# Performance work log

Measured on AMD Instinct MI355X. Metric: run time of the kernel, lower is better.

The kernel has to match this reference:

```python
import jax, jax.numpy as jnp
import numpy as np
import math

B, S, DIM, H = 4, 1024, 4096, 32
HD = DIM // H  # head_dim = 128
MAX_B, MAX_S = 4, 1024
START_POS = 0
ROPE_THETA = 10000.0


def setup_inputs() -> dict:
    key = jax.random.key(0)
    ks = jax.random.split(key, 6)
    x = jax.random.normal(ks[0], (B, S, DIM), dtype=jnp.float32)
    # real RoPE frequencies: freqs_cis[t, j] = exp(i * t * theta^{-2j/hd})
    inv_freq = 1.0 / (ROPE_THETA ** (jnp.arange(0, HD, 2, dtype=jnp.float32) / HD))  # [HD/2]
    t = jnp.arange(START_POS, START_POS + S, dtype=jnp.float32)
    ang = jnp.outer(t, inv_freq)  # [S, HD/2]
    freqs_cos = jnp.cos(ang)
    freqs_sin = jnp.sin(ang)
    # additive causal mask as in llama: -inf above diagonal offset start_pos+1
    mask = jnp.triu(jnp.full((1, 1, S, S), float('-inf'), dtype=jnp.float32), k=START_POS + 1)
    scale = 0.02
    wq = jax.random.normal(ks[1], (DIM, DIM), dtype=jnp.float32) * scale
    wk = jax.random.normal(ks[2], (DIM, DIM), dtype=jnp.float32) * scale
    wv = jax.random.normal(ks[3], (DIM, DIM), dtype=jnp.float32) * scale
    wo = jax.random.normal(ks[4], (DIM, DIM), dtype=jnp.float32) * scale
    cache_k = jnp.zeros((MAX_B, MAX_S, H, HD), dtype=jnp.float32)
    cache_v = jnp.zeros((MAX_B, MAX_S, H, HD), dtype=jnp.float32)
    return {"x": x, "start_pos": START_POS, "freqs_cos": freqs_cos, "freqs_sin": freqs_sin,
            "mask": mask, "wq": wq, "wk": wk, "wv": wv, "wo": wo,
            "cache_k": cache_k, "cache_v": cache_v}


def _apply_rotary(t, cos, sin):
    # t: [B, S, H, HD]; interpret last dim as HD/2 complex pairs (real, imag)
    b, s, h, d = t.shape
    tr = t.reshape(b, s, h, d // 2, 2)
    a, bb = tr[..., 0], tr[..., 1]
    c = cos[None, :, None, :]  # [1, S, 1, HD/2]
    si = sin[None, :, None, :]
    out_r = a * c - bb * si
    out_i = a * si + bb * c
    return jnp.stack([out_r, out_i], axis=-1).reshape(b, s, h, d)


def reference(x, start_pos, freqs_cos, freqs_sin, mask, wq, wk, wv, wo, cache_k, cache_v):
    bsz, seqlen, dim = x.shape
    hd = HD
    # torch Linear: y = x @ W.T, W is [out, in]
    xq = (x @ wq.T).reshape(bsz, seqlen, H, hd)
    xk = (x @ wk.T).reshape(bsz, seqlen, H, hd)
    xv = (x @ wv.T).reshape(bsz, seqlen, H, hd)
    xq = _apply_rotary(xq, freqs_cos, freqs_sin)
    xk = _apply_rotary(xk, freqs_cos, freqs_sin)
    # KV-cache write
    cache_k = jax.lax.dynamic_update_slice(cache_k, xk, (0, start_pos, 0, 0))
    cache_v = jax.lax.dynamic_update_slice(cache_v, xv, (0, start_pos, 0, 0))
    keys = cache_k[:bsz, :start_pos + seqlen]    # [B, K, H, HD]
    values = cache_v[:bsz, :start_pos + seqlen]  # [B, K, H, HD]
    # naive attention: full score matrix
    scores = jnp.einsum('bqhd,bkhd->bhqk', xq, keys) / math.sqrt(hd)
    scores = scores + mask
    probs = jax.nn.softmax(scores.astype(jnp.float32), axis=-1).astype(xq.dtype)
    out = jnp.einsum('bhqk,bkhd->bqhd', probs, values)
    out = out.reshape(bsz, seqlen, -1)
    return out @ wo.T
```

## Files before the change

### kernel.cpp

```cpp
#include <hip/hip_runtime.h>
#include <hip/hip_bf16.h>
#include <cstdint>

typedef __hip_bfloat16 bf16;
typedef __attribute__((ext_vector_type(8))) short frag8;
typedef __attribute__((ext_vector_type(4))) float f32x4;

#define DEV __device__ __forceinline__

DEV void gl_lds16(const void* g, void* l) {
  __builtin_amdgcn_global_load_lds(
      (const __attribute__((address_space(1))) void*)g,
      (__attribute__((address_space(3))) void*)l, 16, 0, 0);
}

DEV void storeC(float* C, size_t idx, float v) { C[idx] = v; }
DEV void storeC(bf16* C, size_t idx, float v) { C[idx] = __float2bfloat16(v); }

__global__ __launch_bounds__(256) void conv_kernel(const float* __restrict__ in,
                                                   bf16* __restrict__ out, int n8) {
  int i = blockIdx.x * 256 + threadIdx.x;
  if (i >= n8) return;
  const float4* in4 = reinterpret_cast<const float4*>(in);
  float4 a = in4[2 * i], b = in4[2 * i + 1];
  union { frag8 v; bf16 h[8]; } u;
  u.h[0] = __float2bfloat16(a.x); u.h[1] = __float2bfloat16(a.y);
  u.h[2] = __float2bfloat16(a.z); u.h[3] = __float2bfloat16(a.w);
  u.h[4] = __float2bfloat16(b.x); u.h[5] = __float2bfloat16(b.y);
  u.h[6] = __float2bfloat16(b.z); u.h[7] = __float2bfloat16(b.w);
  *reinterpret_cast<frag8*>(out + (size_t)i * 8) = u.v;
}

#define MF(a, b, c) __builtin_amdgcn_mfma_f32_16x16x32_bf16(a, b, c, 0, 0, 0)

#define STAGE(isB, h, tt, bp) do {                                             \
    char* _d = lds + ((isB) * 65536) + ((((bp) * 2) + (h)) << 14);             \
    gl_lds16(((isB) ? gB : gA)[h][0] + (size_t)(tt) * 64, _d + ldsOff0);       \
    gl_lds16(((isB) ? gB : gA)[h][1] + (size_t)(tt) * 64, _d + ldsOff1);       \
  } while (0)

#define RDA(mi, ckk) (*(const frag8*)(ab + aRowB + (mi) * 2048 + (ckk)))
#define RDB(ni, ckk) (*(const frag8*)(bb + bRowB + (ni) * 2048 + (ckk)))

#define PHASE(p, SSTAGE, SWAIT) do {                                           \
    if ((p) == 0) {                                                            \
      b00 = RDB(0, ck0); b01 = RDB(0, ck1); b10 = RDB(1, ck0); b11 = RDB(1, ck1); \
      b20 = RDB(2, ck0); b21 = RDB(2, ck1); b30 = RDB(3, ck0); b31 = RDB(3, ck1); \
    }                                                                          \
    frag8 a00 = RDA(2 * (p), ck0), a01 = RDA(2 * (p), ck1);                    \
    frag8 a10 = RDA(2 * (p) + 1, ck0), a11 = RDA(2 * (p) + 1, ck1);            \
    SSTAGE;                                                                    \
    SWAIT;                                                                     \
    __builtin_amdgcn_s_barrier();                                              \
    __builtin_amdgcn_s_setprio(1);                                             \
    acc[2*(p)][0]   = MF(a00, b00, acc[2*(p)][0]);                             \
    acc[2*(p)][1]   = MF(a00, b10, acc[2*(p)][1]);                             \
    acc[2*(p)][2]   = MF(a00, b20, acc[2*(p)][2]);                             \
    acc[2*(p)][3]   = MF(a00, b30, acc[2*(p)][3]);                             \
    acc[2*(p)+1][0] = MF(a10, b00, acc[2*(p)+1][0]);                           \
    acc[2*(p)+1][1] = MF(a10, b10, acc[2*(p)+1][1]);                           \
    acc[2*(p)+1][2] = MF(a10, b20, acc[2*(p)+1][2]);                           \
    acc[2*(p)+1][3] = MF(a10, b30, acc[2*(p)+1][3]);                           \
    acc[2*(p)][0]   = MF(a01, b01, acc[2*(p)][0]);                             \
    acc[2*(p)][1]   = MF(a01, b11, acc[2*(p)][1]);                             \
    acc[2*(p)][2]   = MF(a01, b21, acc[2*(p)][2]);                             \
    acc[2*(p)][3]   = MF(a01, b31, acc[2*(p)][3]);                             \
    acc[2*(p)+1][0] = MF(a11, b01, acc[2*(p)+1][0]);                           \
    acc[2*(p)+1][1] = MF(a11, b11, acc[2*(p)+1][1]);                           \
    acc[2*(p)+1][2] = MF(a11, b21, acc[2*(p)+1][2]);                           \
    acc[2*(p)+1][3] = MF(a11, b31, acc[2*(p)+1][3]);                           \
    __builtin_amdgcn_s_setprio(0);                                             \
    __builtin_amdgcn_s_barrier();                                              \
  } while (0)

#define VM4 asm volatile("s_waitcnt vmcnt(4)" ::: "memory")
#define VM0 asm volatile("s_waitcnt vmcnt(0)" ::: "memory")
#define NOW ((void)0)

#define TILE(t, SA, SB, SWAIT) do {                                            \
    const int _bp2 = ((t) & 1) * 2;                                            \
    char* ab = lds + ((_bp2 + wm) << 14);                                      \
    char* bb = lds + 65536 + ((_bp2 + bhalf) << 14);                           \
    PHASE(0, { if (SA) STAGE(0, 0, (t) + 1, ((t) + 1) & 1); }, NOW);           \
    PHASE(1, { if (SA) STAGE(0, 1, (t) + 1, ((t) + 1) & 1); }, NOW);           \
    PHASE(2, { if (SB) STAGE(1, 0, (t) + 2, (t) & 1); }, NOW);                 \
    PHASE(3, { if (SB) STAGE(1, 1, (t) + 2, (t) & 1); }, SWAIT);               \
  } while (0)

template <typename OutT, int EPI>
__global__ __launch_bounds__(512, 2) void gemm8(const bf16* __restrict__ A,
                                                const bf16* __restrict__ Bt,
                                                OutT* __restrict__ C,
                                                const float* __restrict__ fc,
                                                const float* __restrict__ fs) {
  __shared__ __align__(16) char lds[131072];
  const int K = 4096, N = 4096;
  const int t = threadIdx.x;
  const int lane = t & 63, w = t >> 6;
  const int wm = w >> 2, wn = w & 3;
  const int lr = lane & 15, lg = lane >> 4;
  const int bhalf = wn >> 1;

  const int bid = blockIdx.x;
  const int wg = (bid & 7) * 32 + (bid >> 3);
  const int m0 = (wg >> 4) * 256, n0 = (wg & 15) * 256;

  const bf16* gA[2][2];
  const bf16* gB[2][2];
  int ldsOff0, ldsOff1;
  {
    int c0 = (w * 2 + 0) * 64 + lane;
    int c1 = (w * 2 + 1) * 64 + lane;
    int r0 = c0 >> 3, r1 = c1 >> 3;
    int e0 = ((c0 & 7) ^ (r0 & 7)) * 8;
    int e1 = ((c1 & 7) ^ (r1 & 7)) * 8;
    ldsOff0 = c0 * 16; ldsOff1 = c1 * 16;
    gA[0][0] = A + (size_t)(m0 + r0) * K + e0;
    gA[0][1] = A + (size_t)(m0 + r1) * K + e1;
    gA[1][0] = A + (size_t)(m0 + 128 + r0) * K + e0;
    gA[1][1] = A + (size_t)(m0 + 128 + r1) * K + e1;
    gB[0][0] = Bt + (size_t)(n0 + r0) * K + e0;
    gB[0][1] = Bt + (size_t)(n0 + r1) * K + e1;
    gB[1][0] = Bt + (size_t)(n0 + 128 + r0) * K + e0;
    gB[1][1] = Bt + (size_t)(n0 + 128 + r1) * K + e1;
  }

  const int swz = (lr & 7) << 4;
  const int ck0 = (lg * 16) ^ swz;
  const int ck1 = (64 + lg * 16) ^ swz;
  const int aRowB = lr * 128;
  const int bRowB = ((wn & 1) * 64 + lr) * 128;

  f32x4 acc[8][4];
#pragma unroll
  for (int mi = 0; mi < 8; ++mi)
#pragma unroll
    for (int ni = 0; ni < 4; ++ni) acc[mi][ni] = (f32x4){0.f, 0.f, 0.f, 0.f};

  frag8 b00, b01, b10, b11, b20, b21, b30, b31;

  STAGE(1, 0, 0, 0); STAGE(1, 1, 0, 0);
  STAGE(0, 0, 0, 0); STAGE(0, 1, 0, 0);
  STAGE(1, 0, 1, 1); STAGE(1, 1, 1, 1);
  VM4;
  __builtin_amdgcn_s_barrier();

  for (int tt = 0; tt < 62; tt += 2) {
    TILE(tt, 1, 1, VM4);
    TILE(tt + 1, 1, 1, VM4);
  }
  TILE(62, 1, 0, VM0);
  TILE(63, 0, 0, NOW);

#pragma unroll
  for (int mi = 0; mi < 8; ++mi)
#pragma unroll
    for (int ni = 0; ni < 4; ++ni) {
      f32x4 v = acc[mi][ni];
      int col = n0 + wn * 64 + ni * 16 + lr;
      if (EPI == 1) {
        int i = (col & 127) >> 1;
        const bool odd = (col & 1);
#pragma unroll
        for (int ii = 0; ii < 4; ++ii) {
          int row = m0 + wm * 128 + mi * 16 + lg * 4 + ii;
          int s = row & 1023;
          float c = fc[s * 64 + i], si = fs[s * 64 + i];
          float val = v[ii];
          float par = __shfl_xor(val, 1);
          float o = val * c + (odd ? par * si : -par * si);
          storeC(C, (size_t)row * N + col, o);
        }
      } else if (EPI == 2) {
        int row0 = m0 + wm * 128 + mi * 16 + lg * 4;
        size_t base = ((size_t)(row0 >> 10) * 4096 + col) * 1024 + (row0 & 1023);
        union { ushort4 s4; unsigned short us[4]; } pk;
#pragma unroll
        for (int ii = 0; ii < 4; ++ii) {
          union { bf16 b; unsigned short u; } cv;
          cv.b = __float2bfloat16(v[ii]);
          pk.us[ii] = cv.u;
        }
        *reinterpret_cast<ushort4*>(reinterpret_cast<bf16*>(C) + base) = pk.s4;
      } else {
#pragma unroll
        for (int ii = 0; ii < 4; ++ii) {
          int row = m0 + wm * 128 + mi * 16 + lg * 4 + ii;
          storeC(C, (size_t)row * N + col, v[ii]);
        }
      }
    }
}

__global__ __launch_bounds__(512, 4) void attn_kernel(const bf16* __restrict__ q,
                                                      const bf16* __restrict__ k,
                                                      const bf16* __restrict__ vt,
                                                      bf16* __restrict__ out) {
  __shared__ __align__(16) char als[98304];
  const int qt = blockIdx.x, h = blockIdx.y, b = blockIdx.z;
  const int t = threadIdx.x;
  const int lane = t & 63, w = t >> 6;
  const int lr = lane & 15, lg = lane >> 4;
  const int NT = 2 * qt + 2;

  frag8 aq[4];
  {
    const bf16* qp = q + ((size_t)(b * 1024 + qt * 128 + w * 16 + lr)) * 4096 + h * 128 + lg * 8;
#pragma unroll
    for (int ks = 0; ks < 4; ++ks) aq[ks] = *reinterpret_cast<const frag8*>(qp + ks * 32);
  }

  const bf16* kbase = k + (size_t)b * 1024 * 4096 + h * 128;
  const bf16* vbase = vt + ((size_t)(b * 32 + h)) * 128 * 1024;

  const int L0 = t * 16, L1 = (t + 512) * 16;
  const int kr0 = L0 >> 8, kr1 = L1 >> 8;
  const size_t kOff0 = (size_t)kr0 * 4096 + (((L0 & 255) ^ ((kr0 & 7) << 4)) >> 1);
  const size_t kOff1 = (size_t)kr1 * 4096 + (((L1 & 255) ^ ((kr1 & 7) << 4)) >> 1);
  const int vr0 = L0 >> 7, vr1 = L1 >> 7;
  const size_t vOff0 = (size_t)vr0 * 1024 + (((L0 & 127) ^ ((vr0 & 7) << 4)) >> 1);
  const size_t vOff1 = (size_t)vr1 * 1024 + (((L1 & 127) ^ ((vr1 & 7) << 4)) >> 1);

#define STAGE_K(tt) do { char* _d = als + ((tt) & 1) * 16384;                  \
    gl_lds16(kbase + (size_t)(tt) * 262144 + kOff0, _d + L0);                  \
    gl_lds16(kbase + (size_t)(tt) * 262144 + kOff1, _d + L1); } while (0)
#define STAGE_V(tt) do { char* _d = als + 32768 + ((tt) % 3) * 16384;          \
    gl_lds16(vbase + (size_t)(tt) * 64 + vOff0, _d + L0);                      \
    gl_lds16(vbase + (size_t)(tt) * 64 + vOff1, _d + L1); } while (0)

  f32x4 oacc[8] = {};
  float mrow = -1e30f, lrow = 0.f;
  char* Pw = als + 81920 + w * 2048;
  const float scale = 0.08838834764831845f;
  const int qmaxw = qt * 128 + w * 16 + 15;
  const int qr_g = qt * 128 + w * 16 + lr;

  STAGE_K(0); STAGE_V(0);
  STAGE_K(1); STAGE_V(1);

  for (int kt = 0; kt < NT; ++kt) {
    const bool act = (kt * 64 <= qmaxw);
    const bool domask = (kt >= 2 * qt);
    char* Kc = als + (kt & 1) * 16384;
    char* Vc = als + 32768 + (kt % 3) * 16384;

    if (kt + 1 < NT) { VM4; } else { VM0; }
    __builtin_amdgcn_s_barrier();

    f32x4 sacc[4] = {};
    if (act) {
      __builtin_amdgcn_s_setprio(1);
#pragma unroll
      for (int ks = 0; ks < 4; ++ks) {
#pragma unroll
        for (int ni = 0; ni < 4; ++ni) {
          int n = ni * 16 + lr;
          frag8 bk = *reinterpret_cast<const frag8*>(
              Kc + n * 256 + ((ks * 64 + lg * 16) ^ ((n & 7) << 4)));
          sacc[ni] = MF(bk, aq[ks], sacc[ni]);
        }
      }
      __builtin_amdgcn_s_setprio(0);
    }
    __builtin_amdgcn_s_barrier();
    if (kt + 2 < NT) { STAGE_K(kt + 2); STAGE_V(kt + 2); }

    if (act) {
#pragma unroll
      for (int ni = 0; ni < 4; ++ni)
#pragma unroll
        for (int i = 0; i < 4; ++i) {
          float x = sacc[ni][i] * scale;
          if (domask) {
            int kc = kt * 64 + ni * 16 + lg * 4 + i;
            if (kc > qr_g) x = -1e30f;
          }
          sacc[ni][i] = x;
        }

      float pm = sacc[0][0];
#pragma unroll
      for (int ni = 0; ni < 4; ++ni)
#pragma unroll
        for (int i = 0; i < 4; ++i) pm = fmaxf(pm, sacc[ni][i]);
      pm = fmaxf(pm, __shfl_xor(pm, 16));
      pm = fmaxf(pm, __shfl_xor(pm, 32));
      float mn = fmaxf(mrow, pm);
      float f = __expf(mrow - mn);
      float rs = 0.f;
#pragma unroll
      for (int ni = 0; ni < 4; ++ni)
#pragma unroll
        for (int i = 0; i < 4; ++i) {
          float p = __expf(sacc[ni][i] - mn);
          sacc[ni][i] = p;
          rs += p;
        }
      rs += __shfl_xor(rs, 16);
      rs += __shfl_xor(rs, 32);
      lrow = lrow * f + rs;
      mrow = mn;

#pragma unroll
      for (int ni = 0; ni < 4; ++ni)
#pragma unroll
        for (int jj = 0; jj < 2; ++jj) {
          union { uint32_t u; bf16 hh[2]; } pk;
          pk.hh[0] = __float2bfloat16(sacc[ni][2 * jj]);
          pk.hh[1] = __float2bfloat16(sacc[ni][2 * jj + 1]);
          int kc2 = (ni * 16 + lg * 4 + 2 * jj) * 2;
          *reinterpret_cast<uint32_t*>(Pw + lr * 128 + (kc2 ^ ((lr & 7) << 4))) = pk.u;
        }

      float fi0 = __shfl(f, lg * 4 + 0);
      float fi1 = __shfl(f, lg * 4 + 1);
      float fi2 = __shfl(f, lg * 4 + 2);
      float fi3 = __shfl(f, lg * 4 + 3);
#pragma unroll
      for (int nj = 0; nj < 8; ++nj) {
        oacc[nj][0] *= fi0; oacc[nj][1] *= fi1;
        oacc[nj][2] *= fi2; oacc[nj][3] *= fi3;
      }

      __builtin_amdgcn_s_setprio(1);
#pragma unroll
      for (int ks2 = 0; ks2 < 2; ++ks2) {
        frag8 ap = *reinterpret_cast<const frag8*>(
            Pw + lr * 128 + ((ks2 * 64 + lg * 16) ^ ((lr & 7) << 4)));
#pragma unroll
        for (int nj = 0; nj < 8; ++nj) {
          int d = nj * 16 + lr;
          frag8 bv = *reinterpret_cast<const frag8*>(
              Vc + d * 128 + ((ks2 * 64 + lg * 16) ^ ((d & 7) << 4)));
          oacc[nj] = MF(ap, bv, oacc[nj]);
        }
      }
      __builtin_amdgcn_s_setprio(0);
    }
  }

  float lv0 = __shfl(lrow, lg * 4 + 0);
  float lv1 = __shfl(lrow, lg * 4 + 1);
  float lv2 = __shfl(lrow, lg * 4 + 2);
  float lv3 = __shfl(lrow, lg * 4 + 3);
#pragma unroll
  for (int nj = 0; nj < 8; ++nj) {
    int srow0 = qt * 128 + w * 16 + lg * 4;
    size_t base = ((size_t)(b * 1024 + srow0)) * 4096 + h * 128 + nj * 16 + lr;
    out[base]          = __float2bfloat16(oacc[nj][0] / lv0);
    out[base + 4096]   = __float2bfloat16(oacc[nj][1] / lv1);
    out[base + 8192]   = __float2bfloat16(oacc[nj][2] / lv2);
    out[base + 12288]  = __float2bfloat16(oacc[nj][3] / lv3);
  }
#undef STAGE_K
#undef STAGE_V
}

extern "C" void kernel_launch(void* const* d_in, const int* in_sizes, int n_in,
                              void* d_out, int out_size, void* d_ws, size_t ws_size,
                              hipStream_t stream) {
  const float* x  = (const float*)d_in[0];
  const float* fc = (const float*)d_in[2];
  const float* fs = (const float*)d_in[3];
  const float* wq = (const float*)d_in[5];
  const float* wk = (const float*)d_in[6];
  const float* wv = (const float*)d_in[7];
  const float* wo = (const float*)d_in[8];
  float* out = (float*)d_out;

  const size_t SZ = (size_t)4096 * 4096 * 2;
  char* w = (char*)d_ws;
  bf16* xb  = (bf16*)(w);
  bf16* wb  = (bf16*)(w + SZ);
  bf16* qb  = (bf16*)(w + 2 * SZ);
  bf16* kb  = (bf16*)(w + 3 * SZ);
  bf16* vtb = (bf16*)(w + 4 * SZ);
  bf16* ao  = xb;

  const int n8 = 4096 * 4096 / 8;
  dim3 cgrd(n8 / 256), blk(256);
  dim3 ggrd(256);
  dim3 gblk(512);

  conv_kernel<<<cgrd, blk, 0, stream>>>(x, xb, n8);
  conv_kernel<<<cgrd, blk, 0, stream>>>(wq, wb, n8);
  gemm8<bf16, 1><<<ggrd, gblk, 0, stream>>>(xb, wb, qb, fc, fs);
  conv_kernel<<<cgrd, blk, 0, stream>>>(wk, wb, n8);
  gemm8<bf16, 1><<<ggrd, gblk, 0, stream>>>(xb, wb, kb, fc, fs);
  conv_kernel<<<cgrd, blk, 0, stream>>>(wv, wb, n8);
  gemm8<bf16, 2><<<ggrd, gblk, 0, stream>>>(xb, wb, vtb, fc, fs);
  attn_kernel<<<dim3(8, 32, 4), gblk, 0, stream>>>(qb, kb, vtb, ao);
  conv_kernel<<<cgrd, blk, 0, stream>>>(wo, wb, n8);
  gemm8<float, 0><<<ggrd, gblk, 0, stream>>>(ao, wb, out, fc, fs);
}
```

Measured before the change: 694.6 us.

## Shrink attention query tile to 64 rows and read V directly from global

The attention kernel now uses 256-thread blocks that each handle 64 query rows instead of 128. The grid doubles and LDS per block drops from 96KB to 40KB, which allows higher occupancy and removes the inactive-warp branches on diagonal tiles. V fragments are now loaded straight from global memory inside the PV MFMA loop rather than staged through a triple-buffered LDS tile. This cuts LDS use and staging traffic, at the cost of exposed global-load latency and duplicated V reads across warps and blocks.

Measured after the change: 794.3 us. +14.3%, slower.

```diff
diff --git a/kernel.cpp b/kernel.cpp
--- a/kernel.cpp
+++ b/kernel.cpp
@@ -192,20 +192,20 @@
     }
 }
 
-__global__ __launch_bounds__(512, 4) void attn_kernel(const bf16* __restrict__ q,
+__global__ __launch_bounds__(256, 4) void attn_kernel(const bf16* __restrict__ q,
                                                       const bf16* __restrict__ k,
                                                       const bf16* __restrict__ vt,
                                                       bf16* __restrict__ out) {
-  __shared__ __align__(16) char als[98304];
+  __shared__ __align__(16) char als[40960];
   const int qt = blockIdx.x, h = blockIdx.y, b = blockIdx.z;
   const int t = threadIdx.x;
   const int lane = t & 63, w = t >> 6;
   const int lr = lane & 15, lg = lane >> 4;
-  const int NT = 2 * qt + 2;
+  const int NT = qt + 1;
 
   frag8 aq[4];
   {
-    const bf16* qp = q + ((size_t)(b * 1024 + qt * 128 + w * 16 + lr)) * 4096 + h * 128 + lg * 8;
+    const bf16* qp = q + ((size_t)(b * 1024 + qt * 64 + w * 16 + lr)) * 4096 + h * 128 + lg * 8;
 #pragma unroll
     for (int ks = 0; ks < 4; ++ks) aq[ks] = *reinterpret_cast<const frag8*>(qp + ks * 32);
   }
@@ -213,130 +213,123 @@
   const bf16* kbase = k + (size_t)b * 1024 * 4096 + h * 128;
   const bf16* vbase = vt + ((size_t)(b * 32 + h)) * 128 * 1024;
 
-  const int L0 = t * 16, L1 = (t + 512) * 16;
-  const int kr0 = L0 >> 8, kr1 = L1 >> 8;
-  const size_t kOff0 = (size_t)kr0 * 4096 + (((L0 & 255) ^ ((kr0 & 7) << 4)) >> 1);
-  const size_t kOff1 = (size_t)kr1 * 4096 + (((L1 & 255) ^ ((kr1 & 7) << 4)) >> 1);
-  const int vr0 = L0 >> 7, vr1 = L1 >> 7;
-  const size_t vOff0 = (size_t)vr0 * 1024 + (((L0 & 127) ^ ((vr0 & 7) << 4)) >> 1);
-  const size_t vOff1 = (size_t)vr1 * 1024 + (((L1 & 127) ^ ((vr1 & 7) << 4)) >> 1);
+  size_t kOff[4];
+  int Lc[4];
+#pragma unroll
+  for (int c = 0; c < 4; ++c) {
+    int L = (t + c * 256) * 16;
+    int kr = L >> 8;
+    kOff[c] = (size_t)kr * 4096 + (((L & 255) ^ ((kr & 7) << 4)) >> 1);
+    Lc[c] = L;
+  }
 
 #define STAGE_K(tt) do { char* _d = als + ((tt) & 1) * 16384;                  \
-    gl_lds16(kbase + (size_t)(tt) * 262144 + kOff0, _d + L0);                  \
-    gl_lds16(kbase + (size_t)(tt) * 262144 + kOff1, _d + L1); } while (0)
-#define STAGE_V(tt) do { char* _d = als + 32768 + ((tt) % 3) * 16384;          \
-    gl_lds16(vbase + (size_t)(tt) * 64 + vOff0, _d + L0);                      \
-    gl_lds16(vbase + (size_t)(tt) * 64 + vOff1, _d + L1); } while (0)
+    gl_lds16(kbase + (size_t)(tt) * 262144 + kOff[0], _d + Lc[0]);             \
+    gl_lds16(kbase + (size_t)(tt) * 262144 + kOff[1], _d + Lc[1]);             \
+    gl_lds16(kbase + (size_t)(tt) * 262144 + kOff[2], _d + Lc[2]);             \
+    gl_lds16(kbase + (size_t)(tt) * 262144 + kOff[3], _d + Lc[3]); } while (0)
 
   f32x4 oacc[8] = {};
   float mrow = -1e30f, lrow = 0.f;
-  char* Pw = als + 81920 + w * 2048;
+  char* Pw = als + 32768 + w * 2048;
   const float scale = 0.08838834764831845f;
-  const int qmaxw = qt * 128 + w * 16 + 15;
-  const int qr_g = qt * 128 + w * 16 + lr;
-
-  STAGE_K(0); STAGE_V(0);
-  STAGE_K(1); STAGE_V(1);
+  const int qr_g = qt * 64 + w * 16 + lr;
+
+  STAGE_K(0);
+  STAGE_K(1);
 
   for (int kt = 0; kt < NT; ++kt) {
-    const bool act = (kt * 64 <= qmaxw);
-    const bool domask = (kt >= 2 * qt);
+    const bool domask = (kt == qt);
     char* Kc = als + (kt & 1) * 16384;
-    char* Vc = als + 32768 + (kt % 3) * 16384;
 
     if (kt + 1 < NT) { VM4; } else { VM0; }
     __builtin_amdgcn_s_barrier();
 
     f32x4 sacc[4] = {};
-    if (act) {
-      __builtin_amdgcn_s_setprio(1);
-#pragma unroll
-      for (int ks = 0; ks < 4; ++ks) {
-#pragma unroll
-        for (int ni = 0; ni < 4; ++ni) {
-          int n = ni * 16 + lr;
-          frag8 bk = *reinterpret_cast<const frag8*>(
-              Kc + n * 256 + ((ks * 64 + lg * 16) ^ ((n & 7) << 4)));
-          sacc[ni] = MF(bk, aq[ks], sacc[ni]);
+    __builtin_amdgcn_s_setprio(1);
+#pragma unroll
+    for (int ks = 0; ks < 4; ++ks) {
+#pragma unroll
+      for (int ni = 0; ni < 4; ++ni) {
+        int n = ni * 16 + lr;
+        frag8 bk = *reinterpret_cast<const frag8*>(
+            Kc + n * 256 + ((ks * 64 + lg * 16) ^ ((n & 7) << 4)));
+        sacc[ni] = MF(bk, aq[ks], sacc[ni]);
+      }
+    }
+    __builtin_amdgcn_s_setprio(0);
+    __builtin_amdgcn_s_barrier();
+    if (kt + 2 < NT) STAGE_K(kt + 2);
+
+#pragma unroll
+    for (int ni = 0; ni < 4; ++ni)
+#pragma unroll
+      for (int i = 0; i < 4; ++i) {
+        float x = sacc[ni][i] * scale;
+        if (domask) {
+          int kc = kt * 64 + ni * 16 + lg * 4 + i;
+          if (kc > qr_g) x = -1e30f;
         }
-      }
-      __builtin_amdgcn_s_setprio(0);
+        sacc[ni][i] = x;
+      }
+
+    float pm = sacc[0][0];
+#pragma unroll
+    for (int ni = 0; ni < 4; ++ni)
+#pragma unroll
+      for (int i = 0; i < 4; ++i) pm = fmaxf(pm, sacc[ni][i]);
+    pm = fmaxf(pm, __shfl_xor(pm, 16));
+    pm = fmaxf(pm, __shfl_xor(pm, 32));
+    float mn = fmaxf(mrow, pm);
+    float f = __expf(mrow - mn);
+    float rs = 0.f;
+#pragma unroll
+    for (int ni = 0; ni < 4; ++ni)
+#pragma unroll
+      for (int i = 0; i < 4; ++i) {
+        float p = __expf(sacc[ni][i] - mn);
+        sacc[ni][i] = p;
+        rs += p;
+      }
+    rs += __shfl_xor(rs, 16);
+    rs += __shfl_xor(rs, 32);
+    lrow = lrow * f + rs;
+    mrow = mn;
+
+#pragma unroll
+    for (int ni = 0; ni < 4; ++ni)
+#pragma unroll
+      for (int jj = 0; jj < 2; ++jj) {
+        union { uint32_t u; bf16 hh[2]; } pk;
+        pk.hh[0] = __float2bfloat16(sacc[ni][2 * jj]);
+        pk.hh[1] = __float2bfloat16(sacc[ni][2 * jj + 1]);
+        int kc2 = (ni * 16 + lg * 4 + 2 * jj) * 2;
+        *reinterpret_cast<uint32_t*>(Pw + lr * 128 + (kc2 ^ ((lr & 7) << 4))) = pk.u;
+      }
+
+    float fi0 = __shfl(f, lg * 4 + 0);
+    float fi1 = __shfl(f, lg * 4 + 1);
+    float fi2 = __shfl(f, lg * 4 + 2);
+    float fi3 = __shfl(f, lg * 4 + 3);
+#pragma unroll
+    for (int nj = 0; nj < 8; ++nj) {
+      oacc[nj][0] *= fi0; oacc[nj][1] *= fi1;
+      oacc[nj][2] *= fi2; oacc[nj][3] *= fi3;
     }
-    __builtin_amdgcn_s_barrier();
-    if (kt + 2 < NT) { STAGE_K(kt + 2); STAGE_V(kt + 2); }
-
-    if (act) {
-#pragma unroll
-      for (int ni = 0; ni < 4; ++ni)
-#pragma unroll
-        for (int i = 0; i < 4; ++i) {
-          float x = sacc[ni][i] * scale;
-          if (domask) {
-            int kc = kt * 64 + ni * 16 + lg * 4 + i;
-            if (kc > qr_g) x = -1e30f;
-          }
-          sacc[ni][i] = x;
-        }
-
-      float pm = sacc[0][0];
-#pragma unroll
-      for (int ni = 0; ni < 4; ++ni)
-#pragma unroll
-        for (int i = 0; i < 4; ++i) pm = fmaxf(pm, sacc[ni][i]);
-      pm = fmaxf(pm, __shfl_xor(pm, 16));
-      pm = fmaxf(pm, __shfl_xor(pm, 32));
-      float mn = fmaxf(mrow, pm);
-      float f = __expf(mrow - mn);
-      float rs = 0.f;
-#pragma unroll
-      for (int ni = 0; ni < 4; ++ni)
-#pragma unroll
-        for (int i = 0; i < 4; ++i) {
-          float p = __expf(sacc[ni][i] - mn);
-          sacc[ni][i] = p;
-          rs += p;
-        }
-      rs += __shfl_xor(rs, 16);
-      rs += __shfl_xor(rs, 32);
-      lrow = lrow * f + rs;
-      mrow = mn;
-
-#pragma unroll
-      for (int ni = 0; ni < 4; ++ni)
-#pragma unroll
-        for (int jj = 0; jj < 2; ++jj) {
-          union { uint32_t u; bf16 hh[2]; } pk;
-          pk.hh[0] = __float2bfloat16(sacc[ni][2 * jj]);
-          pk.hh[1] = __float2bfloat16(sacc[ni][2 * jj + 1]);
-          int kc2 = (ni * 16 + lg * 4 + 2 * jj) * 2;
-          *reinterpret_cast<uint32_t*>(Pw + lr * 128 + (kc2 ^ ((lr & 7) << 4))) = pk.u;
-        }
-
-      float fi0 = __shfl(f, lg * 4 + 0);
-      float fi1 = __shfl(f, lg * 4 + 1);
-      float fi2 = __shfl(f, lg * 4 + 2);
-      float fi3 = __shfl(f, lg * 4 + 3);
+
+    __builtin_amdgcn_s_setprio(1);
+#pragma unroll
+    for (int ks2 = 0; ks2 < 2; ++ks2) {
+      frag8 ap = *reinterpret_cast<const frag8*>(
+          Pw + lr * 128 + ((ks2 * 64 + lg * 16) ^ ((lr & 7) << 4)));
 #pragma unroll
       for (int nj = 0; nj < 8; ++nj) {
-        oacc[nj][0] *= fi0; oacc[nj][1] *= fi1;
-        oacc[nj][2] *= fi2; oacc[nj][3] *= fi3;
-      }
-
-      __builtin_amdgcn_s_setprio(1);
-#pragma unroll
-      for (int ks2 = 0; ks2 < 2; ++ks2) {
-        frag8 ap = *reinterpret_cast<const frag8*>(
-            Pw + lr * 128 + ((ks2 * 64 + lg * 16) ^ ((lr & 7) << 4)));
-#pragma unroll
-        for (int nj = 0; nj < 8; ++nj) {
-          int d = nj * 16 + lr;
-          frag8 bv = *reinterpret_cast<const frag8*>(
-              Vc + d * 128 + ((ks2 * 64 + lg * 16) ^ ((d & 7) << 4)));
-          oacc[nj] = MF(ap, bv, oacc[nj]);
-        }
-      }
-      __builtin_amdgcn_s_setprio(0);
+        const bf16* vp = vbase + (size_t)(nj * 16 + lr) * 1024 + kt * 64 + ks2 * 32 + lg * 8;
+        frag8 bv = *reinterpret_cast<const frag8*>(vp);
+        oacc[nj] = MF(ap, bv, oacc[nj]);
+      }
     }
+    __builtin_amdgcn_s_setprio(0);
   }
 
   float lv0 = __shfl(lrow, lg * 4 + 0);
@@ -345,7 +338,7 @@
   float lv3 = __shfl(lrow, lg * 4 + 3);
 #pragma unroll
   for (int nj = 0; nj < 8; ++nj) {
-    int srow0 = qt * 128 + w * 16 + lg * 4;
+    int srow0 = qt * 64 + w * 16 + lg * 4;
     size_t base = ((size_t)(b * 1024 + srow0)) * 4096 + h * 128 + nj * 16 + lr;
     out[base]          = __float2bfloat16(oacc[nj][0] / lv0);
     out[base + 4096]   = __float2bfloat16(oacc[nj][1] / lv1);
@@ -353,7 +346,6 @@
     out[base + 12288]  = __float2bfloat16(oacc[nj][3] / lv3);
   }
 #undef STAGE_K
-#undef STAGE_V
 }
 
 extern "C" void kernel_launch(void* const* d_in, const int* in_sizes, int n_in,
@@ -389,7 +381,7 @@
   gemm8<bf16, 1><<<ggrd, gblk, 0, stream>>>(xb, wb, kb, fc, fs);
   conv_kernel<<<cgrd, blk, 0, stream>>>(wv, wb, n8);
   gemm8<bf16, 2><<<ggrd, gblk, 0, stream>>>(xb, wb, vtb, fc, fs);
-  attn_kernel<<<dim3(8, 32, 4), gblk, 0, stream>>>(qb, kb, vtb, ao);
+  attn_kernel<<<dim3(16, 32, 4), blk, 0, stream>>>(qb, kb, vtb, ao);
   conv_kernel<<<cgrd, blk, 0, stream>>>(wo, wb, n8);
   gemm8<float, 0><<<ggrd, gblk, 0, stream>>>(ao, wb, out, fc, fs);
 }
```

## Fold softmax scale into Q epilogue, lazy rescale, reverse tile order in attention

Applied to the files above, without the earlier changes.

The 1/sqrt(hd) score scale moves into the Q projection's RoPE epilogue, so the attention inner loop no longer multiplies every score. The online softmax skips updating the running max and rescaling the accumulator when no lane's new max exceeds the old one by more than a threshold. This is the lazy-rescale trick and is exact because the final normalisation uses the same stale max. Query tiles launch in reverse order so the longest causal blocks start first. V staging moves from triple to double buffering behind an extra barrier, which frees LDS but adds a synchronisation per iteration.

After: 641.8 us. 1.08x faster.

```diff
diff --git a/kernel.cpp b/kernel.cpp
--- a/kernel.cpp
+++ b/kernel.cpp
@@ -92,7 +92,8 @@
                                                 const bf16* __restrict__ Bt,
                                                 OutT* __restrict__ C,
                                                 const float* __restrict__ fc,
-                                                const float* __restrict__ fs) {
+                                                const float* __restrict__ fs,
+                                                float oscale) {
   __shared__ __align__(16) char lds[131072];
   const int K = 4096, N = 4096;
   const int t = threadIdx.x;
@@ -168,7 +169,7 @@
           float c = fc[s * 64 + i], si = fs[s * 64 + i];
           float val = v[ii];
           float par = __shfl_xor(val, 1);
-          float o = val * c + (odd ? par * si : -par * si);
+          float o = (val * c + (odd ? par * si : -par * si)) * oscale;
           storeC(C, (size_t)row * N + col, o);
         }
       } else if (EPI == 2) {
@@ -196,8 +197,8 @@
                                                       const bf16* __restrict__ k,
                                                       const bf16* __restrict__ vt,
                                                       bf16* __restrict__ out) {
-  __shared__ __align__(16) char als[98304];
-  const int qt = blockIdx.x, h = blockIdx.y, b = blockIdx.z;
+  __shared__ __align__(16) char als[81920];
+  const int qt = 7 - blockIdx.x, h = blockIdx.y, b = blockIdx.z;
   const int t = threadIdx.x;
   const int lane = t & 63, w = t >> 6;
   const int lr = lane & 15, lg = lane >> 4;
@@ -221,28 +222,28 @@
   const size_t vOff0 = (size_t)vr0 * 1024 + (((L0 & 127) ^ ((vr0 & 7) << 4)) >> 1);
   const size_t vOff1 = (size_t)vr1 * 1024 + (((L1 & 127) ^ ((vr1 & 7) << 4)) >> 1);
 
-#define STAGE_K(tt) do { char* _d = als + ((tt) & 1) * 16384;                  \
+#define STAGE_K(tt, bp) do { char* _d = als + (bp) * 16384;                    \
     gl_lds16(kbase + (size_t)(tt) * 262144 + kOff0, _d + L0);                  \
     gl_lds16(kbase + (size_t)(tt) * 262144 + kOff1, _d + L1); } while (0)
-#define STAGE_V(tt) do { char* _d = als + 32768 + ((tt) % 3) * 16384;          \
+#define STAGE_V(tt, bp) do { char* _d = als + 32768 + (bp) * 16384;            \
     gl_lds16(vbase + (size_t)(tt) * 64 + vOff0, _d + L0);                      \
     gl_lds16(vbase + (size_t)(tt) * 64 + vOff1, _d + L1); } while (0)
 
   f32x4 oacc[8] = {};
   float mrow = -1e30f, lrow = 0.f;
-  char* Pw = als + 81920 + w * 2048;
-  const float scale = 0.08838834764831845f;
+  char* Pw = als + 65536 + w * 2048;
   const int qmaxw = qt * 128 + w * 16 + 15;
   const int qr_g = qt * 128 + w * 16 + lr;
 
-  STAGE_K(0); STAGE_V(0);
-  STAGE_K(1); STAGE_V(1);
+  STAGE_K(0, 0); STAGE_V(0, 0);
+  STAGE_K(1, 1); STAGE_V(1, 1);
 
   for (int kt = 0; kt < NT; ++kt) {
+    const int cur = kt & 1;
     const bool act = (kt * 64 <= qmaxw);
     const bool domask = (kt >= 2 * qt);
-    char* Kc = als + (kt & 1) * 16384;
-    char* Vc = als + 32768 + (kt % 3) * 16384;
+    char* Kc = als + cur * 16384;
+    char* Vc = als + 32768 + cur * 16384;
 
     if (kt + 1 < NT) { VM4; } else { VM0; }
     __builtin_amdgcn_s_barrier();
@@ -263,20 +264,18 @@
       __builtin_amdgcn_s_setprio(0);
     }
     __builtin_amdgcn_s_barrier();
-    if (kt + 2 < NT) { STAGE_K(kt + 2); STAGE_V(kt + 2); }
+    if (kt + 2 < NT) STAGE_K(kt + 2, cur);
 
     if (act) {
-#pragma unroll
-      for (int ni = 0; ni < 4; ++ni)
-#pragma unroll
-        for (int i = 0; i < 4; ++i) {
-          float x = sacc[ni][i] * scale;
-          if (domask) {
+      if (domask) {
+#pragma unroll
+        for (int ni = 0; ni < 4; ++ni)
+#pragma unroll
+          for (int i = 0; i < 4; ++i) {
             int kc = kt * 64 + ni * 16 + lg * 4 + i;
-            if (kc > qr_g) x = -1e30f;
+            if (kc > qr_g) sacc[ni][i] = -1e30f;
           }
-          sacc[ni][i] = x;
-        }
+      }
 
       float pm = sacc[0][0];
 #pragma unroll
@@ -285,8 +284,10 @@
         for (int i = 0; i < 4; ++i) pm = fmaxf(pm, sacc[ni][i]);
       pm = fmaxf(pm, __shfl_xor(pm, 16));
       pm = fmaxf(pm, __shfl_xor(pm, 32));
-      float mn = fmaxf(mrow, pm);
-      float f = __expf(mrow - mn);
+      const bool skip = __all(pm <= mrow + 8.f);
+      float mn, f;
+      if (skip) { mn = mrow; f = 1.f; }
+      else      { mn = fmaxf(mrow, pm); f = __expf(mrow - mn); mrow = mn; }
       float rs = 0.f;
 #pragma unroll
       for (int ni = 0; ni < 4; ++ni)
@@ -299,7 +300,6 @@
       rs += __shfl_xor(rs, 16);
       rs += __shfl_xor(rs, 32);
       lrow = lrow * f + rs;
-      mrow = mn;
 
 #pragma unroll
       for (int ni = 0; ni < 4; ++ni)
@@ -312,14 +312,16 @@
           *reinterpret_cast<uint32_t*>(Pw + lr * 128 + (kc2 ^ ((lr & 7) << 4))) = pk.u;
         }
 
-      float fi0 = __shfl(f, lg * 4 + 0);
-      float fi1 = __shfl(f, lg * 4 + 1);
-      float fi2 = __shfl(f, lg * 4 + 2);
-      float fi3 = __shfl(f, lg * 4 + 3);
-#pragma unroll
-      for (int nj = 0; nj < 8; ++nj) {
-        oacc[nj][0] *= fi0; oacc[nj][1] *= fi1;
-        oacc[nj][2] *= fi2; oacc[nj][3] *= fi3;
+      if (!skip) {
+        float fi0 = __shfl(f, lg * 4 + 0);
+        float fi1 = __shfl(f, lg * 4 + 1);
+        float fi2 = __shfl(f, lg * 4 + 2);
+        float fi3 = __shfl(f, lg * 4 + 3);
+#pragma unroll
+        for (int nj = 0; nj < 8; ++nj) {
+          oacc[nj][0] *= fi0; oacc[nj][1] *= fi1;
+          oacc[nj][2] *= fi2; oacc[nj][3] *= fi3;
+        }
       }
 
       __builtin_amdgcn_s_setprio(1);
@@ -337,6 +339,8 @@
       }
       __builtin_amdgcn_s_setprio(0);
     }
+    __builtin_amdgcn_s_barrier();
+    if (kt + 2 < NT) STAGE_V(kt + 2, cur);
   }
 
   float lv0 = __shfl(lrow, lg * 4 + 0);
@@ -384,12 +388,12 @@
 
   conv_kernel<<<cgrd, blk, 0, stream>>>(x, xb, n8);
   conv_kernel<<<cgrd, blk, 0, stream>>>(wq, wb, n8);
-  gemm8<bf16, 1><<<ggrd, gblk, 0, stream>>>(xb, wb, qb, fc, fs);
+  gemm8<bf16, 1><<<ggrd, gblk, 0, stream>>>(xb, wb, qb, fc, fs, 0.08838834764831845f);
   conv_kernel<<<cgrd, blk, 0, stream>>>(wk, wb, n8);
-  gemm8<bf16, 1><<<ggrd, gblk, 0, stream>>>(xb, wb, kb, fc, fs);
+  gemm8<bf16, 1><<<ggrd, gblk, 0, stream>>>(xb, wb, kb, fc, fs, 1.0f);
   conv_kernel<<<cgrd, blk, 0, stream>>>(wv, wb, n8);
-  gemm8<bf16, 2><<<ggrd, gblk, 0, stream>>>(xb, wb, vtb, fc, fs);
+  gemm8<bf16, 2><<<ggrd, gblk, 0, stream>>>(xb, wb, vtb, fc, fs, 1.0f);
   attn_kernel<<<dim3(8, 32, 4), gblk, 0, stream>>>(qb, kb, vtb, ao);
   conv_kernel<<<cgrd, blk, 0, stream>>>(wo, wb, n8);
-  gemm8<float, 0><<<ggrd, gblk, 0, stream>>>(ao, wb, out, fc, fs);
-}
+  gemm8<float, 0><<<ggrd, gblk, 0, stream>>>(ao, wb, out, fc, fs, 1.0f);
+}
```
